# Performance work log

Hardware: AMD Instinct MI355X
Metric: run time of the kernel (lower is better)

## Reference

```python
import jax, jax.numpy as jnp
import numpy as np
from jax import lax

D_MODEL = 512
D_FIBER = 32
D_CONTROL = 64
MOMENTUM = 0.9


def setup_inputs() -> dict:
    key = jax.random.key(0)
    ks = jax.random.split(key, 7)
    B, S = 8, 4096
    hidden = jax.random.normal(ks[0], (B, S, D_MODEL), dtype=jnp.float32)
    # fiber_proj: Linear(d_model -> d_fiber)
    w_fiber = jax.random.normal(ks[1], (D_MODEL, D_FIBER), dtype=jnp.float32) / np.sqrt(D_MODEL)
    b_fiber = jnp.zeros((D_FIBER,), dtype=jnp.float32)
    # predictor: Linear(d_model+d_fiber -> d_control), GELU, Linear(d_control -> 1), Softplus
    w1 = jax.random.normal(ks[2], (D_MODEL + D_FIBER, D_CONTROL), dtype=jnp.float32) / np.sqrt(D_MODEL + D_FIBER)
    b1 = jnp.zeros((D_CONTROL,), dtype=jnp.float32)
    # nn.init.normal_(weight, std=0.01), zero bias for the last linear
    w2 = 0.01 * jax.random.normal(ks[3], (D_CONTROL, 1), dtype=jnp.float32)
    b2 = jnp.zeros((1,), dtype=jnp.float32)
    lambda_gate = jnp.asarray(1.0, dtype=jnp.float32)
    return {"hidden": hidden, "w_fiber": w_fiber, "b_fiber": b_fiber,
            "w1": w1, "b1": b1, "w2": w2, "b2": b2, "lambda_gate": lambda_gate}


def _ema_scan(delta_h, momentum):
    # field_t = momentum * field_{t-1} + (1-momentum) * delta_h_t, field_{-1}=0.
    # Same math as the original full-length causal conv1d (Toeplitz) form,
    # computed in O(S log S) via an associative scan.
    a = jnp.full_like(delta_h, momentum)
    b = (1.0 - momentum) * delta_h

    def combine(c1, c2):
        a1, b1 = c1
        a2, b2 = c2
        return (a1 * a2, a2 * b1 + b2)

    _, field = lax.associative_scan(combine, (a, b), axis=1)
    return field


def reference(hidden, w_fiber, b_fiber, w1, b1, w2, b2, lambda_gate):
    # hidden: [B, S, D]
    fiber = hidden @ w_fiber + b_fiber                      # [B, S, d_fiber]
    combined = jnp.concatenate([hidden, fiber], axis=-1)    # [B, S, D+d_fiber]
    h = jax.nn.gelu(combined @ w1 + b1, approximate=False)  # [B, S, d_control]
    delta_h = jax.nn.softplus((h @ w2 + b2).squeeze(-1))    # [B, S]
    delta_h = jnp.clip(delta_h, 0.0, 1.0)
    field = _ema_scan(delta_h, MOMENTUM)                    # [B, S]
    field = jnp.clip(field, 0.0, 10.0)
    gate = jax.nn.sigmoid(-lambda_gate * field)             # [B, S]
    return (gate, field, delta_h, fiber)
```

## Files before the change

### kernel.cpp

```cpp
#include <hip/hip_runtime.h>
#include <hip/hip_bf16.h>


#define NTOK  32768
#define SEQ   4096
#define DM    512
#define NC    96
#define TB    64
#define KC    256
#define LROW  264

typedef short bf16x8 __attribute__((ext_vector_type(8)));
typedef float f32x4  __attribute__((ext_vector_type(4)));

__device__ __forceinline__ unsigned short f2bf(float f) {
    __hip_bfloat16 h = __float2bfloat16(f);
    return *reinterpret_cast<unsigned short*>(&h);
}

__device__ __forceinline__ bf16x8 cvt8(float4 u, float4 v) {
    bf16x8 r;
    r[0] = (short)f2bf(u.x); r[1] = (short)f2bf(u.y);
    r[2] = (short)f2bf(u.z); r[3] = (short)f2bf(u.w);
    r[4] = (short)f2bf(v.x); r[5] = (short)f2bf(v.y);
    r[6] = (short)f2bf(v.z); r[7] = (short)f2bf(v.w);
    return r;
}

__global__ __launch_bounds__(256)
void prep_kernel(const float* __restrict__ wf,
                 const float* __restrict__ bfb,
                 const float* __restrict__ w1,
                 const float* __restrict__ b1,
                 unsigned short* __restrict__ Wt,
                 float* __restrict__ bc)
{
    int idx = blockIdx.x * 256 + threadIdx.x;
    if (idx < NC * DM) {
        int n = idx >> 9, k = idx & 511;
        float v;
        if (n < 32) {
            v = wf[k * 32 + n];
        } else {
            int c = n - 32;
            v = w1[k * 64 + c];
            const float4* wfr = (const float4*)(wf + k * 32);
#pragma unroll
            for (int f4 = 0; f4 < 8; ++f4) {
                float4 u = wfr[f4];
                v = fmaf(u.x, w1[(512 + f4 * 4 + 0) * 64 + c], v);
                v = fmaf(u.y, w1[(512 + f4 * 4 + 1) * 64 + c], v);
                v = fmaf(u.z, w1[(512 + f4 * 4 + 2) * 64 + c], v);
                v = fmaf(u.w, w1[(512 + f4 * 4 + 3) * 64 + c], v);
            }
        }
        Wt[idx] = f2bf(v);
    }
    if (idx < NC) {
        float v;
        if (idx < 32) {
            v = bfb[idx];
        } else {
            int c = idx - 32;
            v = b1[c];
            for (int f = 0; f < 32; ++f)
                v = fmaf(bfb[f], w1[(512 + f) * 64 + c], v);
        }
        bc[idx] = v;
    }
}

__global__ __launch_bounds__(256, 3)
void fused_gemm_kernel(const float* __restrict__ hidden,
                       const unsigned short* __restrict__ Wt,
                       const float* __restrict__ bc,
                       const float* __restrict__ w2,
                       const float* __restrict__ b2,
                       float* __restrict__ out_delta,
                       float* __restrict__ out_fiber)
{
    __shared__ unsigned short b_lds[NC * LROW];

    const int tid  = threadIdx.x;
    const int wave = tid >> 6;
    const int lane = tid & 63;
    const int quad = lane >> 4;
    const int l15  = lane & 15;
    const int tok0 = blockIdx.x * TB;

    const float* arow = hidden + (size_t)(tok0 + wave * 16 + l15) * DM + quad * 8;

    f32x4 acc[6];
#pragma unroll
    for (int t = 0; t < 6; ++t) acc[t] = (f32x4){0.f, 0.f, 0.f, 0.f};

#pragma unroll
    for (int it = 0; it < 12; ++it) {
        int v   = it * 256 + tid;
        int row = v >> 5;
        int c8  = v & 31;
        bf16x8 u = *(const bf16x8*)(Wt + row * DM + c8 * 8);
        *(bf16x8*)&b_lds[row * LROW + c8 * 8] = u;
    }
    __syncthreads();

    bf16x8 bstage[12];
#pragma unroll
    for (int it = 0; it < 12; ++it) {
        int v   = it * 256 + tid;
        bstage[it] = *(const bf16x8*)(Wt + (v >> 5) * DM + KC + (v & 31) * 8);
    }

#pragma unroll
    for (int ks = 0; ks < 8; ++ks) {
        const float* ap = arow + ks * 32;
        float4 a0 = *(const float4*)ap;
        float4 a1 = *(const float4*)(ap + 4);
        bf16x8 af = cvt8(a0, a1);
#pragma unroll
        for (int t = 0; t < 6; ++t) {
            bf16x8 bfv = *(const bf16x8*)&b_lds[(t * 16 + l15) * LROW + ks * 32 + quad * 8];
            acc[t] = __builtin_amdgcn_mfma_f32_16x16x32_bf16(af, bfv, acc[t], 0, 0, 0);
        }
    }
    __syncthreads();

#pragma unroll
    for (int it = 0; it < 12; ++it) {
        int v = it * 256 + tid;
        *(bf16x8*)&b_lds[(v >> 5) * LROW + (v & 31) * 8] = bstage[it];
    }
    __syncthreads();

#pragma unroll
    for (int ks = 0; ks < 8; ++ks) {
        const float* ap = arow + KC + ks * 32;
        float4 a0 = *(const float4*)ap;
        float4 a1 = *(const float4*)(ap + 4);
        bf16x8 af = cvt8(a0, a1);
#pragma unroll
        for (int t = 0; t < 6; ++t) {
            bf16x8 bfv = *(const bf16x8*)&b_lds[(t * 16 + l15) * LROW + ks * 32 + quad * 8];
            acc[t] = __builtin_amdgcn_mfma_f32_16x16x32_bf16(af, bfv, acc[t], 0, 0, 0);
        }
    }

    const int mbase = tok0 + wave * 16 + quad * 4;

#pragma unroll
    for (int t = 0; t < 2; ++t) {
        int col = t * 16 + l15;
        float bias = bc[col];
#pragma unroll
        for (int r = 0; r < 4; ++r)
            out_fiber[(size_t)(mbase + r) * 32 + col] = acc[t][r] + bias;
    }

    float p0 = 0.f, p1 = 0.f, p2 = 0.f, p3 = 0.f;
#pragma unroll
    for (int t = 2; t < 6; ++t) {
        int c = (t - 2) * 16 + l15;
        float bias = bc[32 + c];
        float w2v  = w2[c];
        float x, g;
        x = acc[t][0] + bias; g = 0.5f * x * (1.f + erff(x * 0.70710678118f)); p0 = fmaf(g, w2v, p0);
        x = acc[t][1] + bias; g = 0.5f * x * (1.f + erff(x * 0.70710678118f)); p1 = fmaf(g, w2v, p1);
        x = acc[t][2] + bias; g = 0.5f * x * (1.f + erff(x * 0.70710678118f)); p2 = fmaf(g, w2v, p2);
        x = acc[t][3] + bias; g = 0.5f * x * (1.f + erff(x * 0.70710678118f)); p3 = fmaf(g, w2v, p3);
    }
#pragma unroll
    for (int m = 1; m <= 8; m <<= 1) {
        p0 += __shfl_xor(p0, m);
        p1 += __shfl_xor(p1, m);
        p2 += __shfl_xor(p2, m);
        p3 += __shfl_xor(p3, m);
    }
    if (l15 < 4) {
        float pv = (l15 == 0) ? p0 : (l15 == 1) ? p1 : (l15 == 2) ? p2 : p3;
        float s = pv + b2[0];
        float d = (s > 0.f) ? s + log1pf(expf(-s)) : log1pf(expf(s));
        d = fminf(fmaxf(d, 0.f), 1.f);
        out_delta[mbase + l15] = d;
    }
}

__global__ __launch_bounds__(256)
void scan_kernel(const float* __restrict__ delta,
                 const float* __restrict__ lam,
                 float* __restrict__ out_gate,
                 float* __restrict__ out_field)
{
    __shared__ float lds_d[384];
    const int b     = blockIdx.x >> 4;
    const int chunk = blockIdx.x & 15;
    const int s0    = chunk * 256;
    const int tid   = threadIdx.x;

    for (int v = tid; v < 384; v += 256) {
        int s = s0 - 128 + v;
        lds_d[v] = (s >= 0) ? delta[b * SEQ + s] : 0.f;
    }
    __syncthreads();

    const int base = 128 + tid;
    const float r4 = 0.6561f;
    float w0 = 0.1f, w1v = 0.09f, w2v = 0.081f, w3v = 0.0729f;
    float p0 = 0.f, p1 = 0.f, p2 = 0.f, p3 = 0.f;
#pragma unroll
    for (int j = 0; j < 128; j += 4) {
        p0 = fmaf(w0,  lds_d[base - j],     p0); w0  *= r4;
        p1 = fmaf(w1v, lds_d[base - j - 1], p1); w1v *= r4;
        p2 = fmaf(w2v, lds_d[base - j - 2], p2); w2v *= r4;
        p3 = fmaf(w3v, lds_d[base - j - 3], p3); w3v *= r4;
    }
    float field = fminf(fmaxf((p0 + p1) + (p2 + p3), 0.f), 10.f);

    float gate = 1.f / (1.f + expf(lam[0] * field));
    int t = b * SEQ + s0 + tid;
    out_field[t] = field;
    out_gate[t]  = gate;
}

extern "C" void kernel_launch(void* const* d_in, const int* in_sizes, int n_in,
                              void* d_out, int out_size, void* d_ws, size_t ws_size,
                              hipStream_t stream)
{
    const float* hidden = (const float*)d_in[0];
    const float* wf     = (const float*)d_in[1];
    const float* bfb    = (const float*)d_in[2];
    const float* w1     = (const float*)d_in[3];
    const float* b1     = (const float*)d_in[4];
    const float* w2     = (const float*)d_in[5];
    const float* b2     = (const float*)d_in[6];
    const float* lam    = (const float*)d_in[7];
    float* out = (float*)d_out;
    float* out_gate  = out;
    float* out_field = out + NTOK;
    float* out_delta = out + 2 * NTOK;
    float* out_fiber = out + 3 * NTOK;

    unsigned short* Wt = (unsigned short*)d_ws;
    float* bc          = (float*)((char*)d_ws + NC * DM * 2);

    hipLaunchKernelGGL(prep_kernel, dim3((NC * DM + 255) / 256), dim3(256), 0, stream,
                       wf, bfb, w1, b1, Wt, bc);
    hipLaunchKernelGGL(fused_gemm_kernel, dim3(NTOK / TB), dim3(256), 0, stream,
                       hidden, Wt, bc, w2, b2, out_delta, out_fiber);
    hipLaunchKernelGGL(scan_kernel, dim3(128), dim3(256), 0, stream,
                       out_delta, lam, out_gate, out_field);
}
```

Baseline: 119.2 us.

## Split fused GEMM output columns across two wave groups per block

Doubles the block to 512 threads so that two groups of four waves share the same 64 tokens, each computing half of the 96 output columns. The partial second-layer dot products are combined through shared memory before the softplus. This halves accumulators and staging registers per wave to raise occupancy and latency hiding. In exchange, each hidden row is loaded twice per block, and the design adds an extra barrier plus a shared-memory reduction.

```diff
diff --git a/kernel.cpp b/kernel.cpp
--- a/kernel.cpp
+++ b/kernel.cpp
@@ -70,7 +70,7 @@
     }
 }
 
-__global__ __launch_bounds__(256, 3)
+__global__ __launch_bounds__(512, 4)
 void fused_gemm_kernel(const float* __restrict__ hidden,
                        const unsigned short* __restrict__ Wt,
                        const float* __restrict__ bc,
@@ -80,23 +80,26 @@
                        float* __restrict__ out_fiber)
 {
     __shared__ unsigned short b_lds[NC * LROW];
-
-    const int tid  = threadIdx.x;
-    const int wave = tid >> 6;
-    const int lane = tid & 63;
-    const int quad = lane >> 4;
-    const int l15  = lane & 15;
-    const int tok0 = blockIdx.x * TB;
-
-    const float* arow = hidden + (size_t)(tok0 + wave * 16 + l15) * DM + quad * 8;
-
-    f32x4 acc[6];
-#pragma unroll
-    for (int t = 0; t < 6; ++t) acc[t] = (f32x4){0.f, 0.f, 0.f, 0.f};
-
-#pragma unroll
-    for (int it = 0; it < 12; ++it) {
-        int v   = it * 256 + tid;
+    __shared__ float part[2][64];
+
+    const int tid   = threadIdx.x;
+    const int wave  = tid >> 6;
+    const int mwave = wave & 3;
+    const int nhalf = wave >> 2;
+    const int lane  = tid & 63;
+    const int quad  = lane >> 4;
+    const int l15   = lane & 15;
+    const int tok0  = blockIdx.x * TB;
+
+    const float* arow = hidden + (size_t)(tok0 + mwave * 16 + l15) * DM + quad * 8;
+
+    f32x4 acc[3];
+#pragma unroll
+    for (int t = 0; t < 3; ++t) acc[t] = (f32x4){0.f, 0.f, 0.f, 0.f};
+
+#pragma unroll
+    for (int it = 0; it < 6; ++it) {
+        int v   = it * 512 + tid;
         int row = v >> 5;
         int c8  = v & 31;
         bf16x8 u = *(const bf16x8*)(Wt + row * DM + c8 * 8);
@@ -104,10 +107,10 @@
     }
     __syncthreads();
 
-    bf16x8 bstage[12];
-#pragma unroll
-    for (int it = 0; it < 12; ++it) {
-        int v   = it * 256 + tid;
+    bf16x8 bstage[6];
+#pragma unroll
+    for (int it = 0; it < 6; ++it) {
+        int v = it * 512 + tid;
         bstage[it] = *(const bf16x8*)(Wt + (v >> 5) * DM + KC + (v & 31) * 8);
     }
 
@@ -118,16 +121,17 @@
         float4 a1 = *(const float4*)(ap + 4);
         bf16x8 af = cvt8(a0, a1);
 #pragma unroll
-        for (int t = 0; t < 6; ++t) {
+        for (int ti = 0; ti < 3; ++ti) {
+            int t = nhalf * 3 + ti;
             bf16x8 bfv = *(const bf16x8*)&b_lds[(t * 16 + l15) * LROW + ks * 32 + quad * 8];
-            acc[t] = __builtin_amdgcn_mfma_f32_16x16x32_bf16(af, bfv, acc[t], 0, 0, 0);
-        }
-    }
-    __syncthreads();
-
-#pragma unroll
-    for (int it = 0; it < 12; ++it) {
-        int v = it * 256 + tid;
+            acc[ti] = __builtin_amdgcn_mfma_f32_16x16x32_bf16(af, bfv, acc[ti], 0, 0, 0);
+        }
+    }
+    __syncthreads();
+
+#pragma unroll
+    for (int it = 0; it < 6; ++it) {
+        int v = it * 512 + tid;
         *(bf16x8*)&b_lds[(v >> 5) * LROW + (v & 31) * 8] = bstage[it];
     }
     __syncthreads();
@@ -139,34 +143,47 @@
         float4 a1 = *(const float4*)(ap + 4);
         bf16x8 af = cvt8(a0, a1);
 #pragma unroll
-        for (int t = 0; t < 6; ++t) {
+        for (int ti = 0; ti < 3; ++ti) {
+            int t = nhalf * 3 + ti;
             bf16x8 bfv = *(const bf16x8*)&b_lds[(t * 16 + l15) * LROW + ks * 32 + quad * 8];
-            acc[t] = __builtin_amdgcn_mfma_f32_16x16x32_bf16(af, bfv, acc[t], 0, 0, 0);
-        }
-    }
-
-    const int mbase = tok0 + wave * 16 + quad * 4;
-
-#pragma unroll
-    for (int t = 0; t < 2; ++t) {
-        int col = t * 16 + l15;
-        float bias = bc[col];
-#pragma unroll
-        for (int r = 0; r < 4; ++r)
-            out_fiber[(size_t)(mbase + r) * 32 + col] = acc[t][r] + bias;
-    }
+            acc[ti] = __builtin_amdgcn_mfma_f32_16x16x32_bf16(af, bfv, acc[ti], 0, 0, 0);
+        }
+    }
+
+    const int mbase = tok0 + mwave * 16 + quad * 4;
 
     float p0 = 0.f, p1 = 0.f, p2 = 0.f, p3 = 0.f;
-#pragma unroll
-    for (int t = 2; t < 6; ++t) {
-        int c = (t - 2) * 16 + l15;
-        float bias = bc[32 + c];
-        float w2v  = w2[c];
-        float x, g;
-        x = acc[t][0] + bias; g = 0.5f * x * (1.f + erff(x * 0.70710678118f)); p0 = fmaf(g, w2v, p0);
-        x = acc[t][1] + bias; g = 0.5f * x * (1.f + erff(x * 0.70710678118f)); p1 = fmaf(g, w2v, p1);
-        x = acc[t][2] + bias; g = 0.5f * x * (1.f + erff(x * 0.70710678118f)); p2 = fmaf(g, w2v, p2);
-        x = acc[t][3] + bias; g = 0.5f * x * (1.f + erff(x * 0.70710678118f)); p3 = fmaf(g, w2v, p3);
+    if (nhalf == 0) {
+#pragma unroll
+        for (int ti = 0; ti < 2; ++ti) {
+            int col = ti * 16 + l15;
+            float bias = bc[col];
+#pragma unroll
+            for (int r = 0; r < 4; ++r)
+                out_fiber[(size_t)(mbase + r) * 32 + col] = acc[ti][r] + bias;
+        }
+        {
+            int c = l15;
+            float bias = bc[32 + c];
+            float w2v  = w2[c];
+            float x, g;
+            x = acc[2][0] + bias; g = 0.5f * x * (1.f + erff(x * 0.70710678118f)); p0 = fmaf(g, w2v, p0);
+            x = acc[2][1] + bias; g = 0.5f * x * (1.f + erff(x * 0.70710678118f)); p1 = fmaf(g, w2v, p1);
+            x = acc[2][2] + bias; g = 0.5f * x * (1.f + erff(x * 0.70710678118f)); p2 = fmaf(g, w2v, p2);
+            x = acc[2][3] + bias; g = 0.5f * x * (1.f + erff(x * 0.70710678118f)); p3 = fmaf(g, w2v, p3);
+        }
+    } else {
+#pragma unroll
+        for (int ti = 0; ti < 3; ++ti) {
+            int c = 16 + ti * 16 + l15;
+            float bias = bc[32 + c];
+            float w2v  = w2[c];
+            float x, g;
+            x = acc[ti][0] + bias; g = 0.5f * x * (1.f + erff(x * 0.70710678118f)); p0 = fmaf(g, w2v, p0);
+            x = acc[ti][1] + bias; g = 0.5f * x * (1.f + erff(x * 0.70710678118f)); p1 = fmaf(g, w2v, p1);
+            x = acc[ti][2] + bias; g = 0.5f * x * (1.f + erff(x * 0.70710678118f)); p2 = fmaf(g, w2v, p2);
+            x = acc[ti][3] + bias; g = 0.5f * x * (1.f + erff(x * 0.70710678118f)); p3 = fmaf(g, w2v, p3);
+        }
     }
 #pragma unroll
     for (int m = 1; m <= 8; m <<= 1) {
@@ -177,10 +194,14 @@
     }
     if (l15 < 4) {
         float pv = (l15 == 0) ? p0 : (l15 == 1) ? p1 : (l15 == 2) ? p2 : p3;
-        float s = pv + b2[0];
+        part[nhalf][mwave * 16 + quad * 4 + l15] = pv;
+    }
+    __syncthreads();
+    if (tid < 64) {
+        float s = part[0][tid] + part[1][tid] + b2[0];
         float d = (s > 0.f) ? s + log1pf(expf(-s)) : log1pf(expf(s));
         d = fminf(fmaxf(d, 0.f), 1.f);
-        out_delta[mbase + l15] = d;
+        out_delta[tok0 + tid] = d;
     }
 }
 
@@ -244,7 +265,7 @@
 
     hipLaunchKernelGGL(prep_kernel, dim3((NC * DM + 255) / 256), dim3(256), 0, stream,
                        wf, bfb, w1, b1, Wt, bc);
-    hipLaunchKernelGGL(fused_gemm_kernel, dim3(NTOK / TB), dim3(256), 0, stream,
+    hipLaunchKernelGGL(fused_gemm_kernel, dim3(NTOK / TB), dim3(512), 0, stream,
                        hidden, Wt, bc, w2, b2, out_delta, out_fiber);
     hipLaunchKernelGGL(scan_kernel, dim3(128), dim3(256), 0, stream,
                        out_delta, lam, out_gate, out_field);
```

After: 122.9 us. 3.0% more time.
